# Kernel tuning notes

Hardware: AMD Instinct MI355X
Metric: run time of the kernel (lower is better)

## Reference

```python
import jax, jax.numpy as jnp
import numpy as np

B, S, H, NH = 8, 4096, 1024, 16
HD = H // NH
EPS_ATTN = 1e-6
EPS_LN = 1e-12


def setup_inputs() -> dict:
    key = jax.random.key(0)
    ks = jax.random.split(key, 10)
    s = 1.0 / np.sqrt(H)
    return {
        "input_tensor": jax.random.normal(ks[0], (B, S, H), dtype=jnp.float32),
        "attention_mask": jnp.zeros((B, S), dtype=jnp.int32),
        "Wq": jax.random.normal(ks[1], (H, H), dtype=jnp.float32) * s,
        "bq": jnp.zeros((H,), dtype=jnp.float32),
        "Wk": jax.random.normal(ks[2], (H, H), dtype=jnp.float32) * s,
        "bk": jnp.zeros((H,), dtype=jnp.float32),
        "Wv": jax.random.normal(ks[3], (H, H), dtype=jnp.float32) * s,
        "bv": jnp.zeros((H,), dtype=jnp.float32),
        "Wd": jax.random.normal(ks[4], (H, H), dtype=jnp.float32) * s,
        "bd": jnp.zeros((H,), dtype=jnp.float32),
        "gamma": jnp.ones((H,), dtype=jnp.float32),
        "beta": jnp.zeros((H,), dtype=jnp.float32),
    }


def reference(input_tensor, attention_mask, Wq, bq, Wk, bk, Wv, bv, Wd, bd, gamma, beta):
    x = input_tensor
    b, s, h = x.shape
    # QKV projections -> [B, S, NH, HD]
    q = (x @ Wq.T + bq).reshape(b, s, NH, HD)
    k = (x @ Wk.T + bk).reshape(b, s, NH, HD)
    v = (x @ Wv.T + bv).reshape(b, s, NH, HD)
    # elu+1 feature map
    q = jax.nn.elu(q) + 1.0
    k = jax.nn.elu(k) + 1.0
    # linear attention: kv state [B, NH, HD_v, HD_k]
    kv = jnp.einsum("nshd,nshm->nhmd", k, v)
    # normalizer: 1 / (q . sum_k)  -> [B, S, NH]
    z = 1.0 / jnp.einsum("nlhd,nhd->nlh", q, k.sum(axis=1) + EPS_ATTN)
    ctx = jnp.einsum("nlhd,nhmd,nlh->nlhm", q, kv, z).reshape(b, s, h)
    # output projection + residual + LayerNorm (dropout is identity in eval)
    hs = ctx @ Wd.T + bd
    hs = hs + x
    mu = hs.mean(axis=-1, keepdims=True)
    var = ((hs - mu) ** 2).mean(axis=-1, keepdims=True)
    out = (hs - mu) / jnp.sqrt(var + EPS_LN) * gamma + beta
    return out
```

## Files before the change

### kernel.cpp

```cpp
#include <hip/hip_runtime.h>
#include <cstdint>
#include <cstddef>

#define BB 8
#define SS 4096
#define HH 1024
#define NHH 16
#define HDD 64
#define MM (BB*SS)
#define KVSPLIT 16

#define BMt 256
#define BNt 256
#define BKt 64
#define NTt (HH/BKt)

typedef __attribute__((ext_vector_type(8))) short short8_t;
typedef __attribute__((ext_vector_type(4))) float f32x4;

__device__ __forceinline__ float bf2f(short u) {
  unsigned int x = ((unsigned int)(unsigned short)u) << 16;
  return __uint_as_float(x);
}
__device__ __forceinline__ short f2bf(float f) {
  unsigned int u = __float_as_uint(f);
  u += 0x7FFFu + ((u >> 16) & 1u);
  return (short)(u >> 16);
}

__device__ __forceinline__ void gload_lds16(const void* g, void* l) {
  __builtin_amdgcn_global_load_lds(
      (const __attribute__((address_space(1))) void*)g,
      (__attribute__((address_space(3))) void*)l, 16, 0, 0);
}

__global__ void cvt_bf16(const float* __restrict__ in, short* __restrict__ out, int n4) {
  int i = blockIdx.x * blockDim.x + threadIdx.x;
  if (i >= n4) return;
  float4 v = ((const float4*)in)[i];
  short4 o;
  o.x = f2bf(v.x); o.y = f2bf(v.y); o.z = f2bf(v.z); o.w = f2bf(v.w);
  ((short4*)out)[i] = o;
}

__device__ __forceinline__ void gemm256_body(
    const short* __restrict__ A, const short* __restrict__ W,
    const float* __restrict__ bias, short* __restrict__ C,
    int m0, int n0, bool act)
{
  __shared__ __align__(16) char smem[131072];

  const int tid  = threadIdx.x;
  const int lane = tid & 63;
  const int wm2  = (tid >> 6) >> 2;
  const int wn   = (tid >> 6) & 3;
  const int fr   = lane & 15;
  const int fg   = lane >> 4;

  const int urow  = tid >> 3;
  const int uslot = tid & 7;
  const short* Asrc = A + (size_t)(m0 + urow) * HH + ((uslot ^ (urow & 7)) << 3);
  const short* Bsrc = W + (size_t)(n0 + urow) * HH + ((uslot ^ (urow & 7)) << 3);
  char* Adst = smem + tid * 16;
  char* Bdst = smem + 65536 + tid * 16;

#define STG_AH(b, kt, h) do { \
    gload_lds16(Asrc + (size_t)((h)*2+0) * 64 * HH + (kt) * 64, Adst + (b) * 32768 + ((h)*2+0) * 8192); \
    gload_lds16(Asrc + (size_t)((h)*2+1) * 64 * HH + (kt) * 64, Adst + (b) * 32768 + ((h)*2+1) * 8192); \
  } while (0)
#define STG_BH(b, kt, h) do { \
    gload_lds16(Bsrc + (size_t)((h)*2+0) * 64 * HH + (kt) * 64, Bdst + (b) * 32768 + ((h)*2+0) * 8192); \
    gload_lds16(Bsrc + (size_t)((h)*2+1) * 64 * HH + (kt) * 64, Bdst + (b) * 32768 + ((h)*2+1) * 8192); \
  } while (0)

  const char* pA = smem + fr * 128;
  const char* pB = smem + 65536 + (wn * 64 + fr) * 128;
  const int sw0 = ((fg)     ^ (fr & 7)) << 4;
  const int sw1 = ((4 + fg) ^ (fr & 7)) << 4;
  const int rowA = wm2 * 8192;

  f32x4 acc[8][4] = {};
  short8_t bfrag[2][4];

  STG_AH(0, 0, 0);
  STG_BH(0, 0, 0);
  STG_BH(0, 0, 1);
  STG_AH(0, 0, 1);
  STG_AH(1, 1, 0);
  STG_BH(1, 1, 0);
  STG_BH(1, 1, 1);
  asm volatile("s_waitcnt vmcnt(8)" ::: "memory");
  __builtin_amdgcn_s_barrier();
  __builtin_amdgcn_sched_barrier(0);

  #pragma unroll 2
  for (int kt = 0; kt < NTt; ++kt) {
    const int buf = kt & 1;
    const int ao = buf * 32768;
    short8_t af[4];

    #pragma unroll
    for (int j = 0; j < 4; j++) bfrag[0][j] = *(const short8_t*)(pB + ao + j * 2048 + sw0);
    #pragma unroll
    for (int i = 0; i < 4; i++) af[i] = *(const short8_t*)(pA + ao + rowA + i * 2048 + sw0);
    if (kt + 1 < NTt) STG_AH(buf ^ 1, kt + 1, 1);
    __builtin_amdgcn_s_barrier();
    __builtin_amdgcn_sched_barrier(0);
    __builtin_amdgcn_s_setprio(1);
    #pragma unroll
    for (int i = 0; i < 4; i++)
      #pragma unroll
      for (int j = 0; j < 4; j++)
        acc[i][j] = __builtin_amdgcn_mfma_f32_16x16x32_bf16(af[i], bfrag[0][j], acc[i][j], 0, 0, 0);
    __builtin_amdgcn_s_setprio(0);
    __builtin_amdgcn_s_barrier();
    __builtin_amdgcn_sched_barrier(0);

    #pragma unroll
    for (int j = 0; j < 4; j++) bfrag[1][j] = *(const short8_t*)(pB + ao + j * 2048 + sw1);
    #pragma unroll
    for (int i = 0; i < 4; i++) af[i] = *(const short8_t*)(pA + ao + rowA + i * 2048 + sw1);
    __builtin_amdgcn_s_barrier();
    __builtin_amdgcn_sched_barrier(0);
    __builtin_amdgcn_s_setprio(1);
    #pragma unroll
    for (int i = 0; i < 4; i++)
      #pragma unroll
      for (int j = 0; j < 4; j++)
        acc[i][j] = __builtin_amdgcn_mfma_f32_16x16x32_bf16(af[i], bfrag[1][j], acc[i][j], 0, 0, 0);
    __builtin_amdgcn_s_setprio(0);
    if (kt < NTt - 2) asm volatile("s_waitcnt vmcnt(8)" ::: "memory");
    else              asm volatile("s_waitcnt vmcnt(0)" ::: "memory");
    __builtin_amdgcn_s_barrier();
    __builtin_amdgcn_sched_barrier(0);

    #pragma unroll
    for (int i = 0; i < 4; i++) af[i] = *(const short8_t*)(pA + ao + 16384 + rowA + i * 2048 + sw0);
    if (kt + 2 < NTt) { STG_AH(buf, kt + 2, 0); STG_BH(buf, kt + 2, 0); }
    __builtin_amdgcn_s_barrier();
    __builtin_amdgcn_sched_barrier(0);
    __builtin_amdgcn_s_setprio(1);
    #pragma unroll
    for (int i = 0; i < 4; i++)
      #pragma unroll
      for (int j = 0; j < 4; j++)
        acc[4 + i][j] = __builtin_amdgcn_mfma_f32_16x16x32_bf16(af[i], bfrag[0][j], acc[4 + i][j], 0, 0, 0);
    __builtin_amdgcn_s_setprio(0);
    __builtin_amdgcn_s_barrier();
    __builtin_amdgcn_sched_barrier(0);

    #pragma unroll
    for (int i = 0; i < 4; i++) af[i] = *(const short8_t*)(pA + ao + 16384 + rowA + i * 2048 + sw1);
    if (kt + 2 < NTt) STG_BH(buf, kt + 2, 1);
    __builtin_amdgcn_s_barrier();
    __builtin_amdgcn_sched_barrier(0);
    __builtin_amdgcn_s_setprio(1);
    #pragma unroll
    for (int i = 0; i < 4; i++)
      #pragma unroll
      for (int j = 0; j < 4; j++)
        acc[4 + i][j] = __builtin_amdgcn_mfma_f32_16x16x32_bf16(af[i], bfrag[1][j], acc[4 + i][j], 0, 0, 0);
    __builtin_amdgcn_s_setprio(0);
    if (kt < NTt - 2) asm volatile("s_waitcnt vmcnt(8)" ::: "memory");
    else              asm volatile("s_waitcnt vmcnt(0)" ::: "memory");
    __builtin_amdgcn_s_barrier();
    __builtin_amdgcn_sched_barrier(0);
  }
#undef STG_AH
#undef STG_BH

  short* sC = (short*)smem;
  float bvj[4];
  #pragma unroll
  for (int j = 0; j < 4; j++) bvj[j] = bias[n0 + wn * 64 + j * 16 + fr];

  #pragma unroll
  for (int h = 0; h < 2; ++h) {
    #pragma unroll
    for (int i = 0; i < 4; i++) {
      #pragma unroll
      for (int j = 0; j < 4; j++) {
        const int col = wn * 64 + j * 16 + fr;
        #pragma unroll
        for (int r = 0; r < 4; r++) {
          float v = acc[h * 4 + i][j][r] + bvj[j];
          if (act) v = (v > 0.f) ? (v + 1.f) : __expf(v);
          sC[(wm2 * 64 + i * 16 + fg * 4 + r) * 264 + col] = f2bf(v);
        }
      }
    }
    __syncthreads();
    const int crow = tid >> 5;
    const int cch  = (tid & 31) * 8;
    #pragma unroll
    for (int p = 0; p < 8; p++) {
      const int row = p * 16 + crow;
      *(short8_t*)(C + (size_t)(m0 + h * 128 + row) * HH + n0 + cch) =
          *(const short8_t*)(sC + row * 264 + cch);
    }
    __syncthreads();
  }
}

__global__ __launch_bounds__(512, 2) void qkv_gemm(
    const short* __restrict__ xb,
    const short* __restrict__ Wqb, const short* __restrict__ Wkb, const short* __restrict__ Wvb,
    const float* __restrict__ bq, const float* __restrict__ bk, const float* __restrict__ bv,
    short* __restrict__ Qo, short* __restrict__ Ko, short* __restrict__ Vo)
{
  const int which = blockIdx.x >> 2;
  const int n0 = (blockIdx.x & 3) * BNt;
  const int m0 = blockIdx.y * BMt;
  const short* W  = (which == 0) ? Wqb : (which == 1) ? Wkb : Wvb;
  const float* bs = (which == 0) ? bq  : (which == 1) ? bk  : bv;
  short* C        = (which == 0) ? Qo  : (which == 1) ? Ko  : Vo;
  gemm256_body(xb, W, bs, C, m0, n0, which < 2);
}

__global__ __launch_bounds__(512, 2) void dproj_gemm(
    const short* __restrict__ A, const short* __restrict__ W,
    const float* __restrict__ bias, short* __restrict__ C)
{
  gemm256_body(A, W, bias, C, blockIdx.y * BMt, blockIdx.x * BNt, false);
}

__global__ __launch_bounds__(256) void kv_part_kernel(
    const short* __restrict__ K_, const short* __restrict__ V_,
    float* __restrict__ kvpart, float* __restrict__ kspart)
{
  __shared__ __align__(16) float sK[32 * 64];
  __shared__ __align__(16) float sV[32 * 64];
  const int h = blockIdx.x, b = blockIdx.y, sp = blockIdx.z;
  const int t = threadIdx.x;
  const int m = t & 63;
  const int dg = (t >> 6) * 16;
  const int lrow = t >> 3;
  const int lcol = (t & 7) * 8;
  const int SC = SS / KVSPLIT;
  float acc[16] = {};
  float ks = 0.f;
  const size_t base = ((size_t)b * SS + (size_t)sp * SC) * HH + (size_t)h * HDD;
  const short* Kp = K_ + base + (size_t)lrow * HH + lcol;
  const short* Vp = V_ + base + (size_t)lrow * HH + lcol;

  for (int sc = 0; sc < SC; sc += 32) {
    short8_t k8 = *(const short8_t*)(Kp + (size_t)sc * HH);
    short8_t v8 = *(const short8_t*)(Vp + (size_t)sc * HH);
    __syncthreads();
    #pragma unroll
    for (int j = 0; j < 8; j++) {
      sK[lrow * 64 + lcol + j] = bf2f(k8[j]);
      sV[lrow * 64 + lcol + j] = bf2f(v8[j]);
    }
    __syncthreads();
    if (t < 64) {
      #pragma unroll
      for (int ss = 0; ss < 32; ss++) ks += sK[ss * 64 + t];
    }
    #pragma unroll 4
    for (int ss = 0; ss < 32; ss++) {
      const float vm = sV[ss * 64 + m];
      const float* kr = sK + ss * 64 + dg;
      #pragma unroll
      for (int j = 0; j < 16; j++) acc[j] += kr[j] * vm;
    }
  }

  const int bh = b * NHH + h;
  float* kvp = kvpart + (size_t)(bh * KVSPLIT + sp) * 4096 + m * 64 + dg;
  #pragma unroll
  for (int j = 0; j < 16; j += 4) {
    f32x4 o;
    o[0] = acc[j]; o[1] = acc[j+1]; o[2] = acc[j+2]; o[3] = acc[j+3];
    *(f32x4*)(kvp + j) = o;
  }
  if (t < 64) kspart[(bh * KVSPLIT + sp) * 64 + t] = ks;
}

__global__ __launch_bounds__(256) void kv_reduce_kernel(
    const float* __restrict__ kvpart, const float* __restrict__ kspart,
    short* __restrict__ kvbf, float* __restrict__ ksum)
{
  const int bh = blockIdx.x;
  const int t = threadIdx.x;
  const float* src = kvpart + (size_t)bh * KVSPLIT * 4096;
  #pragma unroll
  for (int i = 0; i < 4; i++) {
    const int idx = t + i * 256;
    f32x4 s = {};
    #pragma unroll 4
    for (int p = 0; p < KVSPLIT; p++)
      s += ((const f32x4*)(src + (size_t)p * 4096))[idx];
    short4 o;
    o.x = f2bf(s[0]); o.y = f2bf(s[1]); o.z = f2bf(s[2]); o.w = f2bf(s[3]);
    ((short4*)(kvbf + (size_t)bh * 4096))[idx] = o;
  }
  if (t < 64) {
    float s = 0.f;
    #pragma unroll
    for (int p = 0; p < KVSPLIT; p++) s += kspart[(bh * KVSPLIT + p) * 64 + t];
    ksum[bh * 64 + t] = s + 1e-6f;
  }
}

__global__ __launch_bounds__(256) void ctx_mfma(
    const short* __restrict__ Q, const short* __restrict__ kvbf,
    const float* __restrict__ ksum, short* __restrict__ ctx)
{
  __shared__ __align__(16) short sB[64 * 72];
  __shared__ float sks[64];
  __shared__ float sz[256];
  const int b = blockIdx.z, h = blockIdx.y;
  const int t = threadIdx.x;
  const int lane = t & 63, wave = t >> 6;
  const int s0 = blockIdx.x * 256;
  const int bh = b * NHH + h;

  {
    const short8_t* src = (const short8_t*)(kvbf + (size_t)bh * 4096);
    const int m = t >> 2, c = (t & 3) * 16;
    short8_t v0 = src[t * 2], v1 = src[t * 2 + 1];
    *(short8_t*)(sB + m * 72 + c)     = v0;
    *(short8_t*)(sB + m * 72 + c + 8) = v1;
  }
  if (t < 64) sks[t] = ksum[bh * 64 + t];
  __syncthreads();

  {
    const short* qp = Q + (size_t)(b * SS + s0 + t) * HH + h * HDD;
    float zden = 0.f;
    #pragma unroll
    for (int i = 0; i < 8; i++) {
      short8_t q8 = *(const short8_t*)(qp + i * 8);
      #pragma unroll
      for (int j = 0; j < 8; j++) zden += bf2f(q8[j]) * sks[i * 8 + j];
    }
    sz[t] = 1.f / zden;
  }
  __syncthreads();

  const int fr = lane & 15, fk = (lane >> 4) * 8;
  const int wrow = wave * 64;
  f32x4 acc[4][4] = {};
  const short* qbase = Q + (size_t)(b * SS + s0 + wrow + fr) * HH + h * HDD + fk;
  #pragma unroll
  for (int k0 = 0; k0 < 64; k0 += 32) {
    short8_t af[4], wf[4];
    #pragma unroll
    for (int i = 0; i < 4; i++)
      af[i] = *(const short8_t*)(qbase + (size_t)(i * 16) * HH + k0);
    #pragma unroll
    for (int j = 0; j < 4; j++)
      wf[j] = *(const short8_t*)(sB + (j * 16 + fr) * 72 + fk + k0);
    #pragma unroll
    for (int i = 0; i < 4; i++) {
      #pragma unroll
      for (int j = 0; j < 4; j++) {
        acc[i][j] = __builtin_amdgcn_mfma_f32_16x16x32_bf16(af[i], wf[j], acc[i][j], 0, 0, 0);
      }
    }
  }

  const int cr = (lane >> 4) * 4, cc = lane & 15;
  short* cp = ctx + ((size_t)(b * SS + s0)) * HH + h * HDD;
  #pragma unroll
  for (int j = 0; j < 4; j++) {
    const int col = j * 16 + cc;
    #pragma unroll
    for (int i = 0; i < 4; i++) {
      #pragma unroll
      for (int r = 0; r < 4; r++) {
        const int row = wrow + i * 16 + cr + r;
        cp[(size_t)row * HH + col] = f2bf(acc[i][j][r] * sz[row]);
      }
    }
  }
}

__global__ __launch_bounds__(256) void ln_kernel(
    const short* __restrict__ P, const float* __restrict__ x,
    const float* __restrict__ gamma, const float* __restrict__ beta,
    float* __restrict__ out)
{
  const int row = blockIdx.x;
  const int t = threadIdx.x;
  const short* pr = P + (size_t)row * HH;
  const float* xr = x + (size_t)row * HH;
  short4 p4 = ((const short4*)pr)[t];
  float4 x4 = ((const float4*)xr)[t];
  float h0 = bf2f(p4.x) + x4.x;
  float h1 = bf2f(p4.y) + x4.y;
  float h2 = bf2f(p4.z) + x4.z;
  float h3 = bf2f(p4.w) + x4.w;
  float s1 = h0 + h1 + h2 + h3;
  float s2 = h0*h0 + h1*h1 + h2*h2 + h3*h3;
  #pragma unroll
  for (int o = 32; o > 0; o >>= 1) {
    s1 += __shfl_xor(s1, o);
    s2 += __shfl_xor(s2, o);
  }
  __shared__ float red[8];
  const int wv = t >> 6, ln = t & 63;
  if (ln == 0) { red[wv] = s1; red[4 + wv] = s2; }
  __syncthreads();
  const float S1 = red[0] + red[1] + red[2] + red[3];
  const float S2 = red[4] + red[5] + red[6] + red[7];
  const float mu  = S1 * (1.f / HH);
  const float var = S2 * (1.f / HH) - mu * mu;
  const float inv = rsqrtf(var + 1e-12f);
  float4 g4 = ((const float4*)gamma)[t];
  float4 b4 = ((const float4*)beta)[t];
  float4 o4;
  o4.x = (h0 - mu) * inv * g4.x + b4.x;
  o4.y = (h1 - mu) * inv * g4.y + b4.y;
  o4.z = (h2 - mu) * inv * g4.z + b4.z;
  o4.w = (h3 - mu) * inv * g4.w + b4.w;
  ((float4*)(out + (size_t)row * HH))[t] = o4;
}

extern "C" void kernel_launch(void* const* d_in, const int* in_sizes, int n_in,
                              void* d_out, int out_size, void* d_ws, size_t ws_size,
                              hipStream_t stream)
{
  const float* x     = (const float*)d_in[0];
  const float* Wq    = (const float*)d_in[2];
  const float* bq    = (const float*)d_in[3];
  const float* Wk    = (const float*)d_in[4];
  const float* bk    = (const float*)d_in[5];
  const float* Wv    = (const float*)d_in[6];
  const float* bv    = (const float*)d_in[7];
  const float* Wd    = (const float*)d_in[8];
  const float* bd    = (const float*)d_in[9];
  const float* gamma = (const float*)d_in[10];
  const float* beta  = (const float*)d_in[11];
  float* out = (float*)d_out;

  char* ws = (char*)d_ws;
  const size_t MB64 = 67108864;
  short* xb  = (short*)(ws + 0 * MB64);
  short* Qb  = (short*)(ws + 1 * MB64);
  short* Kb  = (short*)(ws + 2 * MB64);
  short* Vb  = (short*)(ws + 3 * MB64);
  short* Cb  = (short*)(ws + 4 * MB64);
  short* Wqb = (short*)(ws + 5 * MB64 + 0 * 2097152);
  short* Wkb = (short*)(ws + 5 * MB64 + 1 * 2097152);
  short* Wvb = (short*)(ws + 5 * MB64 + 2 * 2097152);
  short* Wdb = (short*)(ws + 5 * MB64 + 3 * 2097152);
  short* kvbf= (short*)(ws + 5 * MB64 + 4 * 2097152);
  float* ksb = (float*)(ws + 5 * MB64 + 5 * 2097152);
  float* kvpart = (float*)(ws + 4 * MB64);
  float* kspart = kvpart + (size_t)128 * KVSPLIT * 4096;
  short* Pb  = Qb;

  cvt_bf16<<<(MM * HH / 4) / 256, 256, 0, stream>>>(x,  xb,  MM * HH / 4);
  cvt_bf16<<<(HH * HH / 4) / 256, 256, 0, stream>>>(Wq, Wqb, HH * HH / 4);
  cvt_bf16<<<(HH * HH / 4) / 256, 256, 0, stream>>>(Wk, Wkb, HH * HH / 4);
  cvt_bf16<<<(HH * HH / 4) / 256, 256, 0, stream>>>(Wv, Wvb, HH * HH / 4);
  cvt_bf16<<<(HH * HH / 4) / 256, 256, 0, stream>>>(Wd, Wdb, HH * HH / 4);

  qkv_gemm<<<dim3(12, MM / BMt), 512, 0, stream>>>(xb, Wqb, Wkb, Wvb, bq, bk, bv, Qb, Kb, Vb);

  kv_part_kernel<<<dim3(NHH, BB, KVSPLIT), 256, 0, stream>>>(Kb, Vb, kvpart, kspart);
  kv_reduce_kernel<<<BB * NHH, 256, 0, stream>>>(kvpart, kspart, kvbf, ksb);
  ctx_mfma<<<dim3(SS / 256, NHH, BB), 256, 0, stream>>>(Qb, kvbf, ksb, Cb);

  dproj_gemm<<<dim3(HH / BNt, MM / BMt), 512, 0, stream>>>(Cb, Wdb, bd, Pb);
  ln_kernel<<<MM, 256, 0, stream>>>(Pb, x, gamma, beta, out);
}
```

Before: 721.2 us.

## Software-pipeline LDS fragment reads one stage ahead of MFMA in GEMM main loop

Restructures the 256x256 bf16 GEMM main loop so LDS reads for the next MFMA quarter are issued before the current quarter's MFMAs. Explicit lgkmcnt waits replace full barrier-waits, and the last two k-tiles are peeled into an epilogue. The goal is to hide LDS read latency behind MFMA work and drop some barriers. In exchange it uses double register fragments for A and B, which raises register pressure at 2 waves/SIMD, and the hand-tuned waitcnt counts risk subtle hazards.

```diff
diff --git a/kernel.cpp b/kernel.cpp
--- a/kernel.cpp
+++ b/kernel.cpp
@@ -79,92 +79,114 @@
   const int sw1 = ((4 + fg) ^ (fr & 7)) << 4;
   const int rowA = wm2 * 8192;
 
+#define DSR_A(RA, OFS, SW) do { \
+    _Pragma("unroll") \
+    for (int i_ = 0; i_ < 4; i_++) (RA)[i_] = *(const short8_t*)(pA + (OFS) + i_ * 2048 + (SW)); \
+  } while (0)
+#define DSR_B(RB, OFS, SW) do { \
+    _Pragma("unroll") \
+    for (int j_ = 0; j_ < 4; j_++) (RB)[j_] = *(const short8_t*)(pB + (OFS) + j_ * 2048 + (SW)); \
+  } while (0)
+#define MFMA16(OFS, RA, RB) do { \
+    _Pragma("unroll") \
+    for (int i_ = 0; i_ < 4; i_++) { \
+      _Pragma("unroll") \
+      for (int j_ = 0; j_ < 4; j_++) \
+        acc[(OFS) + i_][j_] = __builtin_amdgcn_mfma_f32_16x16x32_bf16((RA)[i_], (RB)[j_], acc[(OFS) + i_][j_], 0, 0, 0); \
+    } \
+  } while (0)
+#define LGKM8() asm volatile("s_waitcnt lgkmcnt(8)" ::: "memory")
+#define LGKM4() asm volatile("s_waitcnt lgkmcnt(4)" ::: "memory")
+#define LGKM0() asm volatile("s_waitcnt lgkmcnt(0)" ::: "memory")
+#define SBAR()  __builtin_amdgcn_s_barrier()
+#define SCHED() __builtin_amdgcn_sched_barrier(0)
+#define PRIO1() __builtin_amdgcn_s_setprio(1)
+#define PRIO0() __builtin_amdgcn_s_setprio(0)
+
   f32x4 acc[8][4] = {};
-  short8_t bfrag[2][4];
-
-  STG_AH(0, 0, 0);
-  STG_BH(0, 0, 0);
-  STG_BH(0, 0, 1);
-  STG_AH(0, 0, 1);
-  STG_AH(1, 1, 0);
-  STG_BH(1, 1, 0);
-  STG_BH(1, 1, 1);
+  short8_t RA0[4], RA1[4], RB0[4], RB1[4];
+
+  STG_AH(0, 0, 0); STG_BH(0, 0, 0); STG_BH(0, 0, 1);
+  SCHED();
+  STG_AH(0, 0, 1); STG_AH(1, 1, 0); STG_BH(1, 1, 0); STG_BH(1, 1, 1);
   asm volatile("s_waitcnt vmcnt(8)" ::: "memory");
-  __builtin_amdgcn_s_barrier();
-  __builtin_amdgcn_sched_barrier(0);
+  SBAR(); SCHED();
+  DSR_B(RB0, 0, sw0);
+  DSR_A(RA0, rowA, sw0);
 
   #pragma unroll 2
-  for (int kt = 0; kt < NTt; ++kt) {
-    const int buf = kt & 1;
-    const int ao = buf * 32768;
-    short8_t af[4];
-
-    #pragma unroll
-    for (int j = 0; j < 4; j++) bfrag[0][j] = *(const short8_t*)(pB + ao + j * 2048 + sw0);
-    #pragma unroll
-    for (int i = 0; i < 4; i++) af[i] = *(const short8_t*)(pA + ao + rowA + i * 2048 + sw0);
-    if (kt + 1 < NTt) STG_AH(buf ^ 1, kt + 1, 1);
-    __builtin_amdgcn_s_barrier();
-    __builtin_amdgcn_sched_barrier(0);
-    __builtin_amdgcn_s_setprio(1);
-    #pragma unroll
-    for (int i = 0; i < 4; i++)
-      #pragma unroll
-      for (int j = 0; j < 4; j++)
-        acc[i][j] = __builtin_amdgcn_mfma_f32_16x16x32_bf16(af[i], bfrag[0][j], acc[i][j], 0, 0, 0);
-    __builtin_amdgcn_s_setprio(0);
-    __builtin_amdgcn_s_barrier();
-    __builtin_amdgcn_sched_barrier(0);
-
-    #pragma unroll
-    for (int j = 0; j < 4; j++) bfrag[1][j] = *(const short8_t*)(pB + ao + j * 2048 + sw1);
-    #pragma unroll
-    for (int i = 0; i < 4; i++) af[i] = *(const short8_t*)(pA + ao + rowA + i * 2048 + sw1);
-    __builtin_amdgcn_s_barrier();
-    __builtin_amdgcn_sched_barrier(0);
-    __builtin_amdgcn_s_setprio(1);
-    #pragma unroll
-    for (int i = 0; i < 4; i++)
-      #pragma unroll
-      for (int j = 0; j < 4; j++)
-        acc[i][j] = __builtin_amdgcn_mfma_f32_16x16x32_bf16(af[i], bfrag[1][j], acc[i][j], 0, 0, 0);
-    __builtin_amdgcn_s_setprio(0);
-    if (kt < NTt - 2) asm volatile("s_waitcnt vmcnt(8)" ::: "memory");
-    else              asm volatile("s_waitcnt vmcnt(0)" ::: "memory");
-    __builtin_amdgcn_s_barrier();
-    __builtin_amdgcn_sched_barrier(0);
-
-    #pragma unroll
-    for (int i = 0; i < 4; i++) af[i] = *(const short8_t*)(pA + ao + 16384 + rowA + i * 2048 + sw0);
-    if (kt + 2 < NTt) { STG_AH(buf, kt + 2, 0); STG_BH(buf, kt + 2, 0); }
-    __builtin_amdgcn_s_barrier();
-    __builtin_amdgcn_sched_barrier(0);
-    __builtin_amdgcn_s_setprio(1);
-    #pragma unroll
-    for (int i = 0; i < 4; i++)
-      #pragma unroll
-      for (int j = 0; j < 4; j++)
-        acc[4 + i][j] = __builtin_amdgcn_mfma_f32_16x16x32_bf16(af[i], bfrag[0][j], acc[4 + i][j], 0, 0, 0);
-    __builtin_amdgcn_s_setprio(0);
-    __builtin_amdgcn_s_barrier();
-    __builtin_amdgcn_sched_barrier(0);
-
-    #pragma unroll
-    for (int i = 0; i < 4; i++) af[i] = *(const short8_t*)(pA + ao + 16384 + rowA + i * 2048 + sw1);
-    if (kt + 2 < NTt) STG_BH(buf, kt + 2, 1);
-    __builtin_amdgcn_s_barrier();
-    __builtin_amdgcn_sched_barrier(0);
-    __builtin_amdgcn_s_setprio(1);
-    #pragma unroll
-    for (int i = 0; i < 4; i++)
-      #pragma unroll
-      for (int j = 0; j < 4; j++)
-        acc[4 + i][j] = __builtin_amdgcn_mfma_f32_16x16x32_bf16(af[i], bfrag[1][j], acc[4 + i][j], 0, 0, 0);
-    __builtin_amdgcn_s_setprio(0);
-    if (kt < NTt - 2) asm volatile("s_waitcnt vmcnt(8)" ::: "memory");
-    else              asm volatile("s_waitcnt vmcnt(0)" ::: "memory");
-    __builtin_amdgcn_s_barrier();
-    __builtin_amdgcn_sched_barrier(0);
+  for (int kt = 0; kt < NTt - 2; ++kt) {
+    const int ao = (kt & 1) * 32768;
+    const int an = ao ^ 32768;
+    DSR_B(RB1, ao, sw1);
+    DSR_A(RA1, ao + rowA, sw1);
+    STG_AH((kt & 1) ^ 1, kt + 1, 1);
+    LGKM8(); SCHED();
+    PRIO1(); MFMA16(0, RA0, RB0); PRIO0();
+    asm volatile("s_waitcnt vmcnt(8)" ::: "memory");
+    SBAR(); SCHED();
+    DSR_A(RA0, ao + 16384 + rowA, sw0);
+    LGKM4(); SCHED();
+    PRIO1(); MFMA16(0, RA1, RB1); PRIO0();
+    SBAR(); SCHED();
+    DSR_A(RA1, ao + 16384 + rowA, sw1);
+    STG_AH(kt & 1, kt + 2, 0); STG_BH(kt & 1, kt + 2, 0);
+    LGKM4(); SCHED();
+    PRIO1(); MFMA16(4, RA0, RB0); PRIO0();
+    asm volatile("s_waitcnt vmcnt(6)" ::: "memory");
+    SBAR(); SCHED();
+    DSR_B(RB0, an, sw0);
+    DSR_A(RA0, an + rowA, sw0);
+    STG_BH(kt & 1, kt + 2, 1);
+    LGKM8(); SCHED();
+    PRIO1(); MFMA16(4, RA1, RB1); PRIO0();
+    SBAR(); SCHED();
+  }
+
+  {
+    const int ao = ((NTt - 2) & 1) * 32768;
+    const int an = ao ^ 32768;
+    DSR_B(RB1, ao, sw1);
+    DSR_A(RA1, ao + rowA, sw1);
+    STG_AH(((NTt - 2) & 1) ^ 1, NTt - 1, 1);
+    LGKM8(); SCHED();
+    PRIO1(); MFMA16(0, RA0, RB0); PRIO0();
+    asm volatile("s_waitcnt vmcnt(8)" ::: "memory");
+    SBAR(); SCHED();
+    DSR_A(RA0, ao + 16384 + rowA, sw0);
+    LGKM4(); SCHED();
+    PRIO1(); MFMA16(0, RA1, RB1); PRIO0();
+    SBAR(); SCHED();
+    DSR_A(RA1, ao + 16384 + rowA, sw1);
+    LGKM4(); SCHED();
+    PRIO1(); MFMA16(4, RA0, RB0); PRIO0();
+    asm volatile("s_waitcnt vmcnt(2)" ::: "memory");
+    SBAR(); SCHED();
+    DSR_B(RB0, an, sw0);
+    DSR_A(RA0, an + rowA, sw0);
+    LGKM8(); SCHED();
+    PRIO1(); MFMA16(4, RA1, RB1); PRIO0();
+    SBAR(); SCHED();
+  }
+  {
+    const int ao = ((NTt - 1) & 1) * 32768;
+    DSR_B(RB1, ao, sw1);
+    DSR_A(RA1, ao + rowA, sw1);
+    LGKM8(); SCHED();
+    PRIO1(); MFMA16(0, RA0, RB0); PRIO0();
+    asm volatile("s_waitcnt vmcnt(0)" ::: "memory");
+    SBAR(); SCHED();
+    DSR_A(RA0, ao + 16384 + rowA, sw0);
+    LGKM4(); SCHED();
+    PRIO1(); MFMA16(0, RA1, RB1); PRIO0();
+    SBAR(); SCHED();
+    DSR_A(RA1, ao + 16384 + rowA, sw1);
+    LGKM4(); SCHED();
+    PRIO1(); MFMA16(4, RA0, RB0); PRIO0();
+    SBAR(); SCHED();
+    LGKM0(); SCHED();
+    PRIO1(); MFMA16(4, RA1, RB1); PRIO0();
+    SBAR(); SCHED();
   }
 #undef STG_AH
 #undef STG_BH
@@ -200,6 +222,16 @@
     }
     __syncthreads();
   }
+#undef DSR_A
+#undef DSR_B
+#undef MFMA16
+#undef LGKM8
+#undef LGKM4
+#undef LGKM0
+#undef SBAR
+#undef SCHED
+#undef PRIO1
+#undef PRIO0
 }
 
 __global__ __launch_bounds__(512, 2) void qkv_gemm(
```

Result: no change. 710.7 us (-1.5%).
